# Kernel optimization log

Measured on AMD Instinct MI355X. Metric: run time of the kernel, lower is better.

Reference implementation:

```python
import jax, jax.numpy as jnp
import numpy as np

BETA = 0.04
EPS_LOW = 0.2
EPS_HIGH = 0.2
TEMPERATURE = 1.0


def setup_inputs() -> dict:
    key = jax.random.key(0)
    ks = jax.random.split(key, 8)
    B, S, H, V = 4, 1024, 2048, 32000
    return {
        "_input": jax.random.normal(ks[0], (B, S, H), dtype=jnp.float32),
        "lin_weight": jax.random.normal(ks[1], (V, H), dtype=jnp.float32) * 0.02,
        "bias": jax.random.normal(ks[2], (V,), dtype=jnp.float32) * 0.02,
        "selected_token_ids": jax.random.randint(ks[3], (B, S), 0, V),
        "attention_mask": jnp.ones((B, S), dtype=jnp.float32),
        "advantages": jax.random.normal(ks[4], (B,), dtype=jnp.float32),
        "ref_per_token_logps": -jnp.abs(jax.random.normal(ks[5], (B, S), dtype=jnp.float32)),
        "old_per_token_logps": -jnp.abs(jax.random.normal(ks[6], (B, S), dtype=jnp.float32)),
    }


def reference(_input, lin_weight, bias, selected_token_ids, attention_mask,
              advantages, ref_per_token_logps, old_per_token_logps):
    B, S, H = _input.shape
    # fused linear projection to vocab logits: [B,S,V]
    logits = (jnp.einsum("bsh,vh->bsv", _input, lin_weight) + bias) / TEMPERATURE
    log_probs = jax.nn.log_softmax(logits, axis=-1)
    per_token_logps = jnp.take_along_axis(
        log_probs, selected_token_ids[..., None], axis=-1)[..., 0]  # [B,S]

    log_ratio = per_token_logps - old_per_token_logps
    seq_len = jnp.clip(attention_mask.sum(-1), 1.0, None)
    seq_level_log_weight = jax.lax.stop_gradient(
        (log_ratio * attention_mask).sum(-1) / seq_len)[:, None]  # [B,1]

    log_importance_weights = (per_token_logps -
                              jax.lax.stop_gradient(per_token_logps) +
                              seq_level_log_weight)
    coef_1 = jnp.exp(log_importance_weights)
    coef_2 = jnp.clip(coef_1, 1.0 - EPS_LOW, 1.0 + EPS_HIGH)
    adv = advantages[:, None]
    per_token_loss = -jnp.minimum(coef_1 * adv, coef_2 * adv)

    # k3 KL penalty (beta != 0, use_ref_model=True)
    d = ref_per_token_logps - per_token_logps
    kl_div = jnp.exp(d) - d - 1.0
    per_token_loss = per_token_loss + BETA * kl_div

    # loss_type == 'grpo'
    loss = ((per_token_loss * attention_mask).sum(-1) / seq_len).sum() / B
    return loss
```

## Files before the change

### kernel.cpp

```cpp
#include <hip/hip_runtime.h>
#include <hip/hip_bf16.h>

#define BETA_C 0.04f
#define EPS_LOW_C 0.2f
#define EPS_HIGH_C 0.2f

static constexpr int B_ = 4, S_ = 1024, H_ = 2048, V_ = 32000;
static constexpr int M_ = B_ * S_;
static constexpr int BM = 256, BN = 256, BK = 64;
static constexpr int NRB = M_ / BM;
static constexpr int NCB = V_ / BN;
static constexpr int NT  = H_ / BK;

typedef __attribute__((ext_vector_type(8))) short short8;
typedef __attribute__((ext_vector_type(4))) float f32x4;

__device__ __forceinline__ unsigned short f2bf(float f) {
    unsigned u = __builtin_bit_cast(unsigned, f);
    unsigned r = 0x7FFFu + ((u >> 16) & 1u);
    return (unsigned short)((u + r) >> 16);
}

__device__ __forceinline__ void gload_lds16(const unsigned short* g, unsigned short* l) {
    __builtin_amdgcn_global_load_lds(
        (const __attribute__((address_space(1))) unsigned int*)g,
        (__attribute__((address_space(3))) unsigned int*)l, 16, 0, 0);
}

__global__ void cvt_kernel(const float* __restrict__ in, unsigned short* __restrict__ out, int n4) {
    int i = blockIdx.x * blockDim.x + threadIdx.x;
    int stride = gridDim.x * blockDim.x;
    for (; i < n4; i += stride) {
        float4 v = reinterpret_cast<const float4*>(in)[i];
        ushort4 o;
        o.x = f2bf(v.x); o.y = f2bf(v.y); o.z = f2bf(v.z); o.w = f2bf(v.w);
        reinterpret_cast<ushort4*>(out)[i] = o;
    }
}

__global__ __launch_bounds__(512, 2) void gemm_lse_kernel(
    const unsigned short* __restrict__ A,
    const unsigned short* __restrict__ W,
    const float* __restrict__ bias,
    const int* __restrict__ sel,
    float* __restrict__ partials,
    float* __restrict__ sel_logit)
{
    __shared__ __attribute__((aligned(128))) char lds[163840];

    const int bid = blockIdx.x;
    const int swz = (bid & 7) * (NRB * NCB / 8) + (bid >> 3);
    const int brow = swz % NRB;
    const int bcol = swz / NRB;
    const int tid  = threadIdx.x;
    const int lane = tid & 63;
    const int wv   = tid >> 6;
    const int wm   = wv >> 2;
    const int wn   = wv & 3;
    const int l15  = lane & 15, lg = lane >> 4;

    int aBase[2], bBase[2];
    #pragma unroll
    for (int ks = 0; ks < 2; ++ks) {
        const int sw = ((ks * 4 + lg) ^ (l15 & 7)) << 4;
        aBase[ks] = (wm * 128 + l15) * 128 + sw;
        bBase[ks] = (wn * 64 + l15) * 128 + sw;
    }
    int sByte[2][2];
    #pragma unroll
    for (int i = 0; i < 2; ++i)
        #pragma unroll
        for (int h = 0; h < 2; ++h) {
            int c = i * 512 + tid;
            int r = (c >> 3) + h * 128;
            int gg = (c & 7) ^ (r & 7);
            sByte[i][h] = (r * H_ + gg * 8) * 2;
        }

    const unsigned short* Ab = A + (long)brow * BM * H_;
    const unsigned short* Wb = W + (long)bcol * BN * H_;

    f32x4 acc[8][4] = {};
    short8 af[2][2], bfr[4][2];

#define STG(gb, bufoff, h, kt) \
    { _Pragma("unroll") \
      for (int i_ = 0; i_ < 2; ++i_) \
          gload_lds16((const unsigned short*)((const char*)(gb) + sByte[i_][h] + (kt) * 2), \
                      (unsigned short*)(lds + (bufoff) + (h) * 16384 + (i_ * 512 + tid) * 16)); }

#define RDA(abuf, q) \
    { _Pragma("unroll") \
      for (int mi_ = 0; mi_ < 2; ++mi_) \
      _Pragma("unroll") \
      for (int ks_ = 0; ks_ < 2; ++ks_) \
          af[mi_][ks_] = *(const short8*)(lds + (abuf) + ((q) * 2 + mi_) * 2048 + aBase[ks_]); }

#define RDB(bbuf) \
    { _Pragma("unroll") \
      for (int n_ = 0; n_ < 4; ++n_) \
      _Pragma("unroll") \
      for (int ks_ = 0; ks_ < 2; ++ks_) \
          bfr[n_][ks_] = *(const short8*)(lds + (bbuf) + n_ * 2048 + bBase[ks_]); }

#define MM(q) \
    __builtin_amdgcn_s_setprio(1); \
    _Pragma("unroll") \
    for (int ks_ = 0; ks_ < 2; ++ks_) \
    _Pragma("unroll") \
    for (int mi_ = 0; mi_ < 2; ++mi_) \
    _Pragma("unroll") \
    for (int n_ = 0; n_ < 4; ++n_) \
        acc[(q) * 2 + mi_][n_] = __builtin_amdgcn_mfma_f32_16x16x32_bf16( \
            af[mi_][ks_], bfr[n_][ks_], acc[(q) * 2 + mi_][n_], 0, 0, 0); \
    __builtin_amdgcn_s_setprio(0);

#define LGKM(n) asm volatile("s_waitcnt lgkmcnt(" #n ")" ::: "memory");
#define LGKM0   asm volatile("s_waitcnt lgkmcnt(0)" ::: "memory"); \
    __builtin_amdgcn_sched_barrier(0);
#define VMC(n)  asm volatile("s_waitcnt vmcnt(" #n ")" ::: "memory");
#define BAR     { __builtin_amdgcn_s_barrier(); __builtin_amdgcn_sched_barrier(0); }

    STG(Ab, 0, 0, 0)       STG(Ab, 0, 1, 0)
    STG(Wb, 65536, 0, 0)   STG(Wb, 65536, 1, 0)
    STG(Wb, 98304, 0, 64)  STG(Wb, 98304, 1, 64)
    VMC(4)
    BAR

    #pragma unroll
    for (int t = 0; t < NT; ++t) {
        const int aR = (t & 1) * 32768;
        const int aW = ((t + 1) & 1) * 32768;
        const int bR = 65536 + (t % 3) * 32768;
        const int bW = 65536 + ((t + 2) % 3) * 32768;
        const int ktA = ((t + 1) * BK) & (H_ - 1);
        const int ktB = ((t + 2) * BK) & (H_ - 1);

        RDB(bR) RDA(aR, 0)
        STG(Ab, aW, 0, ktA)
        LGKM(8)
        BAR
        LGKM0
        MM(0)
        BAR
        RDA(aR, 1)
        STG(Ab, aW, 1, ktA)
        BAR
        LGKM0
        MM(1)
        BAR
        RDA(aR, 2)
        STG(Wb, bW, 0, ktB)
        BAR
        LGKM0
        MM(2)
        BAR
        RDA(aR, 3)
        STG(Wb, bW, 1, ktB)
        VMC(4)
        BAR
        LGKM0
        MM(3)
        BAR
    }

    VMC(0)
    __syncthreads();

    float* sums = (float*)lds;
    const int colb = bcol * BN + wn * 64 + l15;
    float bv[4];
    #pragma unroll
    for (int n = 0; n < 4; ++n) bv[n] = bias[colb + n * 16];

    #pragma unroll
    for (int m = 0; m < 8; ++m) {
        #pragma unroll
        for (int j = 0; j < 4; ++j) {
            const long grow = (long)brow * BM + wm * 128 + m * 16 + lg * 4 + j;
            const int stok = sel[grow];
            float s = 0.f;
            #pragma unroll
            for (int n = 0; n < 4; ++n) {
                float logit = acc[m][n][j] + bv[n];
                s += __expf(logit);
                if (stok == colb + n * 16) sel_logit[grow] = logit;
            }
            s += __shfl_xor(s, 1); s += __shfl_xor(s, 2);
            s += __shfl_xor(s, 4); s += __shfl_xor(s, 8);
            if (l15 == 0) sums[(wm * 128 + m * 16 + lg * 4 + j) * 4 + wn] = s;
        }
    }
    __syncthreads();
    if (tid < BM) {
        float tot = sums[tid * 4 + 0] + sums[tid * 4 + 1] + sums[tid * 4 + 2] + sums[tid * 4 + 3];
        partials[((long)brow * BM + tid) * NCB + bcol] = tot;
    }
#undef STG
#undef RDA
#undef RDB
#undef MM
#undef LGKM
#undef LGKM0
#undef VMC
#undef BAR
}

__global__ void reduce_lse_kernel(const float* __restrict__ partials,
                                  const float* __restrict__ sel_logit,
                                  float* __restrict__ lp) {
    const int row = blockIdx.x;
    const int lane = threadIdx.x;
    float s = 0.f;
    for (int i = lane; i < NCB; i += 64) s += partials[(long)row * NCB + i];
    #pragma unroll
    for (int o = 32; o; o >>= 1) s += __shfl_xor(s, o);
    if (lane == 0) lp[row] = sel_logit[row] - __logf(s);
}

__device__ __forceinline__ float block_sum(float v, float* red) {
    const int lane = threadIdx.x & 63, wid = threadIdx.x >> 6;
    #pragma unroll
    for (int o = 32; o; o >>= 1) v += __shfl_xor(v, o);
    if (lane == 0) red[wid] = v;
    __syncthreads();
    if (wid == 0) {
        float x = (lane < 16) ? red[lane] : 0.f;
        #pragma unroll
        for (int o = 8; o; o >>= 1) x += __shfl_xor(x, o);
        if (lane == 0) red[0] = x;
    }
    __syncthreads();
    float r = red[0];
    __syncthreads();
    return r;
}

__global__ __launch_bounds__(1024) void loss_kernel(
    const float* __restrict__ lp, const float* __restrict__ mask,
    const float* __restrict__ adv, const float* __restrict__ ref,
    const float* __restrict__ old, float* __restrict__ out) {
    __shared__ float red[16];
    const int s = threadIdx.x;
    float loss_acc = 0.f;
    for (int b = 0; b < 4; ++b) {
        const int i = b * S_ + s;
        const float mk = mask[i];
        const float lpv = lp[i];
        const float lrsum = block_sum((lpv - old[i]) * mk, red);
        const float msum  = block_sum(mk, red);
        const float seqlen = fmaxf(msum, 1.f);
        const float sw = lrsum / seqlen;
        const float c1 = __expf(sw);
        const float c2 = fminf(fmaxf(c1, 1.f - EPS_LOW_C), 1.f + EPS_HIGH_C);
        const float a = adv[b];
        const float pmin = fminf(c1 * a, c2 * a);
        const float d = ref[i] - lpv;
        const float ptl = -pmin + BETA_C * (__expf(d) - d - 1.f);
        const float lsum = block_sum(ptl * mk, red);
        loss_acc += lsum / seqlen;
    }
    if (s == 0) out[0] = loss_acc * (1.f / (float)B_);
}

extern "C" void kernel_launch(void* const* d_in, const int* in_sizes, int n_in,
                              void* d_out, int out_size, void* d_ws, size_t ws_size,
                              hipStream_t stream) {
    const float* x    = (const float*)d_in[0];
    const float* W    = (const float*)d_in[1];
    const float* bias = (const float*)d_in[2];
    const int*   sel  = (const int*)d_in[3];
    const float* mask = (const float*)d_in[4];
    const float* adv  = (const float*)d_in[5];
    const float* ref  = (const float*)d_in[6];
    const float* old  = (const float*)d_in[7];
    float* out = (float*)d_out;

    char* ws = (char*)d_ws;
    unsigned short* Abf = (unsigned short*)ws;
    unsigned short* Wbf = (unsigned short*)(ws + 16777216);
    float* partials  = (float*)(ws + 16777216 + 131072000);
    float* sel_logit = (float*)(ws + 16777216 + 131072000 + 2048000);
    float* lp        = sel_logit + M_;

    cvt_kernel<<<2048, 256, 0, stream>>>(x, Abf, M_ * H_ / 4);
    cvt_kernel<<<4096, 256, 0, stream>>>(W, Wbf, V_ * H_ / 4);

    gemm_lse_kernel<<<NRB * NCB, 512, 0, stream>>>(Abf, Wbf, bias, sel, partials, sel_logit);

    reduce_lse_kernel<<<M_, 64, 0, stream>>>(partials, sel_logit, lp);
    loss_kernel<<<1, 1024, 0, stream>>>(lp, mask, adv, ref, old, out);
}
```

Before: 554.3 us.

## Restructure GEMM k-loop to one barrier per step with register-buffered A fragments

The main k-loop of the fused logits GEMM moves from four barrier-separated phases to a single end-of-step barrier. All global-to-LDS stage loads for the next tiles are issued at the start of the step. A fragments now go into four separate register sets, so LDS reads for later quarter-tiles overlap the MFMAs of earlier ones, gated by lgkmcnt waits and scheduling barriers. This cuts barrier stalls and exposes more LDS/MFMA overlap, at the cost of more VGPRs, which may lower occupancy or cause spills.

New measurement: 554.7 us. No clear change (+0.1%).

```diff
diff --git a/kernel.cpp b/kernel.cpp
--- a/kernel.cpp
+++ b/kernel.cpp
@@ -81,7 +81,7 @@
     const unsigned short* Wb = W + (long)bcol * BN * H_;
 
     f32x4 acc[8][4] = {};
-    short8 af[2][2], bfr[4][2];
+    short8 af0[2][2], af1[2][2], af2[2][2], af3[2][2], bfr[4][2];
 
 #define STG(gb, bufoff, h, kt) \
     { _Pragma("unroll") \
@@ -89,12 +89,12 @@
           gload_lds16((const unsigned short*)((const char*)(gb) + sByte[i_][h] + (kt) * 2), \
                       (unsigned short*)(lds + (bufoff) + (h) * 16384 + (i_ * 512 + tid) * 16)); }
 
-#define RDA(abuf, q) \
+#define RDA(abuf, q, dst) \
     { _Pragma("unroll") \
       for (int mi_ = 0; mi_ < 2; ++mi_) \
       _Pragma("unroll") \
       for (int ks_ = 0; ks_ < 2; ++ks_) \
-          af[mi_][ks_] = *(const short8*)(lds + (abuf) + ((q) * 2 + mi_) * 2048 + aBase[ks_]); }
+          dst[mi_][ks_] = *(const short8*)(lds + (abuf) + ((q) * 2 + mi_) * 2048 + aBase[ks_]); }
 
 #define RDB(bbuf) \
     { _Pragma("unroll") \
@@ -103,7 +103,7 @@
       for (int ks_ = 0; ks_ < 2; ++ks_) \
           bfr[n_][ks_] = *(const short8*)(lds + (bbuf) + n_ * 2048 + bBase[ks_]); }
 
-#define MM(q) \
+#define MM(q, afr) \
     __builtin_amdgcn_s_setprio(1); \
     _Pragma("unroll") \
     for (int ks_ = 0; ks_ < 2; ++ks_) \
@@ -112,14 +112,14 @@
     _Pragma("unroll") \
     for (int n_ = 0; n_ < 4; ++n_) \
         acc[(q) * 2 + mi_][n_] = __builtin_amdgcn_mfma_f32_16x16x32_bf16( \
-            af[mi_][ks_], bfr[n_][ks_], acc[(q) * 2 + mi_][n_], 0, 0, 0); \
+            afr[mi_][ks_], bfr[n_][ks_], acc[(q) * 2 + mi_][n_], 0, 0, 0); \
     __builtin_amdgcn_s_setprio(0);
 
-#define LGKM(n) asm volatile("s_waitcnt lgkmcnt(" #n ")" ::: "memory");
-#define LGKM0   asm volatile("s_waitcnt lgkmcnt(0)" ::: "memory"); \
+#define LGKM(n) asm volatile("s_waitcnt lgkmcnt(" #n ")" ::: "memory"); \
     __builtin_amdgcn_sched_barrier(0);
 #define VMC(n)  asm volatile("s_waitcnt vmcnt(" #n ")" ::: "memory");
 #define BAR     { __builtin_amdgcn_s_barrier(); __builtin_amdgcn_sched_barrier(0); }
+#define SCB     __builtin_amdgcn_sched_barrier(0);
 
     STG(Ab, 0, 0, 0)       STG(Ab, 0, 1, 0)
     STG(Wb, 65536, 0, 0)   STG(Wb, 65536, 1, 0)
@@ -136,31 +136,25 @@
         const int ktA = ((t + 1) * BK) & (H_ - 1);
         const int ktB = ((t + 2) * BK) & (H_ - 1);
 
-        RDB(bR) RDA(aR, 0)
-        STG(Ab, aW, 0, ktA)
-        LGKM(8)
-        BAR
-        LGKM0
-        MM(0)
-        BAR
-        RDA(aR, 1)
-        STG(Ab, aW, 1, ktA)
-        BAR
-        LGKM0
-        MM(1)
-        BAR
-        RDA(aR, 2)
-        STG(Wb, bW, 0, ktB)
-        BAR
-        LGKM0
-        MM(2)
-        BAR
-        RDA(aR, 3)
-        STG(Wb, bW, 1, ktB)
+        RDB(bR) RDA(aR, 0, af0)
+        SCB
+        RDA(aR, 1, af1)
+        SCB
+        STG(Ab, aW, 0, ktA) STG(Ab, aW, 1, ktA)
+        STG(Wb, bW, 0, ktB) STG(Wb, bW, 1, ktB)
+        LGKM(4)
+        MM(0, af0)
+        RDA(aR, 2, af2)
+        SCB
+        LGKM(4)
+        MM(1, af1)
+        RDA(aR, 3, af3)
+        SCB
+        LGKM(4)
+        MM(2, af2)
+        LGKM(0)
+        MM(3, af3)
         VMC(4)
-        BAR
-        LGKM0
-        MM(3)
         BAR
     }
 
@@ -201,9 +195,9 @@
 #undef RDB
 #undef MM
 #undef LGKM
-#undef LGKM0
 #undef VMC
 #undef BAR
+#undef SCB
 }
 
 __global__ void reduce_lse_kernel(const float* __restrict__ partials,
```
